# Kernel tuning notes

Measured on AMD Instinct MI355X. Metric: run time of the kernel, lower is better.

Reference implementation:

```python
import jax, jax.numpy as jnp
import numpy as np

B, S, IN = 1024, 256, 8
H = 512
F = 96  # forecast_len
OUT = 1


def _lstm_step(h, c, x, Wih, Whh, bih, bhh):
    # PyTorch gate order: i, f, g, o
    gates = x @ Wih.T + h @ Whh.T + (bih + bhh)  # [B, 4H]
    i, f, g, o = jnp.split(gates, 4, axis=-1)
    i = jax.nn.sigmoid(i)
    f = jax.nn.sigmoid(f)
    g = jnp.tanh(g)
    o = jax.nn.sigmoid(o)
    c_new = f * c + i * g
    h_new = o * jnp.tanh(c_new)
    return h_new, c_new


def setup_inputs() -> dict:
    key = jax.random.key(0)
    ks = jax.random.split(key, 12)
    s_in = 1.0 / np.sqrt(H)
    def u(k, shape):
        return jax.random.uniform(k, shape, jnp.float32, -s_in, s_in)
    return {
        "x": jax.random.normal(ks[0], (B, S, IN), jnp.float32),
        "enc_Wih": u(ks[1], (4 * H, IN)),
        "enc_Whh": u(ks[2], (4 * H, H)),
        "enc_bih": u(ks[3], (4 * H,)),
        "enc_bhh": u(ks[4], (4 * H,)),
        "dec_Wih": u(ks[5], (4 * H, OUT)),
        "dec_Whh": u(ks[6], (4 * H, H)),
        "dec_bih": u(ks[7], (4 * H,)),
        "dec_bhh": u(ks[8], (4 * H,)),
        "out_W": u(ks[9], (OUT, H)),
        "out_b": u(ks[10], (OUT,)),
    }


def reference(x, enc_Wih, enc_Whh, enc_bih, enc_bhh,
              dec_Wih, dec_Whh, dec_bih, dec_bhh, out_W, out_b):
    batch = x.shape[0]
    h0 = jnp.zeros((batch, H), x.dtype)
    c0 = jnp.zeros((batch, H), x.dtype)

    # ---- Encoder: scan over time ----
    def enc_step(carry, xt):
        h, c = carry
        h, c = _lstm_step(h, c, xt, enc_Wih, enc_Whh, enc_bih, enc_bhh)
        return (h, c), None

    xs = jnp.swapaxes(x, 0, 1)  # [S, B, IN]
    (h, c), _ = jax.lax.scan(enc_step, (h0, c0), xs)

    y0 = jnp.zeros((batch, OUT), x.dtype)

    def dec_step(carry, _):
        h, c, y = carry
        h, c = _lstm_step(h, c, y, dec_Wih, dec_Whh, dec_bih, dec_bhh)
        pred = h @ out_W.T + out_b  # [B, 1]
        return (h, c, pred), pred

    _, preds = jax.lax.scan(dec_step, (h, c, y0), None, length=F)  # [F, B, 1]
    return jnp.swapaxes(preds[..., 0], 0, 1)  # [B, F]
```

## Files before the change

kernel.cpp:

```cpp
#include <hip/hip_runtime.h>


#define Hh 512
#define K2 544
#define BATCH 1024
#define SEQ 256
#define FCAST 96
#define Mrows 64
#define SAS 552
#define SHS 40

typedef _Float16 f16;
typedef _Float16 f16x8 __attribute__((ext_vector_type(8)));
typedef float f32x4 __attribute__((ext_vector_type(4)));

__device__ __forceinline__ float sigf(float v) { return 1.0f / (1.0f + __expf(-v)); }
__device__ __forceinline__ float tanhf_(float v) { return 1.0f - 2.0f / (__expf(2.0f * v) + 1.0f); }

__device__ __forceinline__ f16x8 ld16(const f16* p, bool byp) {
  f16x8 d;
  if (byp) asm volatile("global_load_dwordx4 %0, %1, off sc0 sc1" : "=v"(d) : "v"(p) : "memory");
  else     asm volatile("global_load_dwordx4 %0, %1, off sc0"     : "=v"(d) : "v"(p) : "memory");
  return d;
}
__device__ __forceinline__ void st16(f16* p, f16x8 v, bool byp) {
  if (byp) asm volatile("global_store_dwordx4 %0, %1, off sc0 sc1" :: "v"(p), "v"(v) : "memory");
  else     asm volatile("global_store_dwordx4 %0, %1, off"         :: "v"(p), "v"(v) : "memory");
}
__device__ __forceinline__ int atomic_add_l2(int* p, int v) {
  int old;
  asm volatile("global_atomic_add %0, %1, %2, off sc0\n\ts_waitcnt vmcnt(0)"
               : "=v"(old) : "v"(p), "v"(v) : "memory");
  return old;
}

__global__ void prep_weights(const float* __restrict__ encWih, const float* __restrict__ encWhh,
                             const float* __restrict__ decWih, const float* __restrict__ decWhh,
                             const float* __restrict__ encBih, const float* __restrict__ encBhh,
                             const float* __restrict__ decBih, const float* __restrict__ decBhh,
                             const float* __restrict__ outW, const float* __restrict__ outB,
                             f16* __restrict__ encT, f16* __restrict__ decPW, f16* __restrict__ decFW,
                             float* __restrict__ bE, float* __restrict__ bP, float* __restrict__ bF) {
  int id = blockIdx.x * 256 + threadIdx.x;
  if (id >= 2048 * 68) return;
  int n = id / 68, c8 = id % 68;
  int nslot = n >> 7, c = n & 127, w = c >> 5, cc = c & 31, ct = cc >> 4, l4v = cc & 15;
  int g = ct * 2 + (l4v >> 3), j = l4v & 7;
  int unit = nslot * 32 + w * 8 + j, r = g * Hh + unit;
  size_t o = (size_t)n * K2 + c8 * 8;
  if (c8 < 64) {
    float dwih = decWih[r];
#pragma unroll
    for (int e = 0; e < 8; ++e) {
      int k = c8 * 8 + e;
      encT[o + e] = (f16)encWhh[(size_t)r * Hh + k];
      float dw = decWhh[(size_t)r * Hh + k];
      decPW[o + e] = (f16)dw;
      decFW[o + e] = (f16)(dw + outW[k] * dwih);
    }
  } else if (c8 == 64) {
#pragma unroll
    for (int e = 0; e < 8; ++e) {
      encT[o + e] = (f16)encWih[r * 8 + e];
      decPW[o + e] = (f16)0.f;
      decFW[o + e] = (f16)0.f;
    }
  } else {
#pragma unroll
    for (int e = 0; e < 8; ++e) {
      encT[o + e] = (f16)0.f;
      decPW[o + e] = (f16)0.f;
      decFW[o + e] = (f16)0.f;
    }
  }
  if (c8 == 0) {
    bE[n] = encBih[r] + encBhh[r];
    float bd = decBih[r] + decBhh[r];
    bP[n] = bd;
    bF[n] = bd + outB[0] * decWih[r];
  }
}

__global__ void init_state(f16* __restrict__ h0, float* __restrict__ out,
                           const float* __restrict__ outB, int* __restrict__ sync) {
  int i = blockIdx.x * 256 + threadIdx.x;
  if (i < BATCH * Hh) h0[i] = (f16)0.f;
  if (i < BATCH * FCAST) out[i] = outB[0];
  if (i < 2048) sync[i] = 0;
}

__global__ __launch_bounds__(256, 1) void lstm_persist(
    const f16* __restrict__ encT, const f16* __restrict__ decPW, const f16* __restrict__ decFW,
    const float* __restrict__ bE, const float* __restrict__ bP, const float* __restrict__ bF,
    const float* __restrict__ x, f16* __restrict__ h0, f16* __restrict__ h1,
    float* __restrict__ out, const float* __restrict__ outW, int* __restrict__ sync) {
  __shared__ __align__(16) f16 sA[Mrows * SAS];
  __shared__ __align__(16) f16 sH[Mrows * SHS];
  __shared__ int sInfo[2];

  int* cnt = sync;
  int* slots = sync + 1024;
  int* arrive = sync + 1032;

  const int T = threadIdx.x;
  const int w = T >> 6, lane = T & 63, l4 = lane & 15, q = lane >> 4;
  const int j = l4 & 7;
  const bool lo = (l4 < 8);

  int xcd;
  asm("s_getreg_b32 %0, hwreg(HW_REG_XCC_ID)" : "=s"(xcd));
  xcd &= 7;

  if (T == 0) {
    int r = __hip_atomic_fetch_add(&slots[xcd], 1, __ATOMIC_RELAXED, __HIP_MEMORY_SCOPE_AGENT);
    sInfo[0] = r;
    __hip_atomic_fetch_add(arrive, 1, __ATOMIC_RELAXED, __HIP_MEMORY_SCOPE_AGENT);
    while (__hip_atomic_load(arrive, __ATOMIC_RELAXED, __HIP_MEMORY_SCOPE_AGENT) < 256)
      __builtin_amdgcn_s_sleep(2);
    int ok = 1;
    for (int xx = 0; xx < 8; ++xx)
      ok &= (__hip_atomic_load(&slots[xx], __ATOMIC_RELAXED, __HIP_MEMORY_SCOPE_AGENT) == 32);
    sInfo[1] = ok;
  }
  __syncthreads();
  const int rank = sInfo[0];
  const bool uni = (sInfo[1] != 0);
  int group, nslot;
  if (uni) { group = xcd * 2 + (rank >> 4); nslot = rank & 15; }
  else     { group = (int)blockIdx.x >> 4;  nslot = (int)blockIdx.x & 15; }
  const int m0 = group * Mrows, n0 = nslot * 128, u0 = nslot * 32;
  int* myCnt = cnt + group * 32;

  f16x8 bw[2][17];
  float bias_r[4];
  float cst[2][4];
#pragma unroll
  for (int a = 0; a < 2; ++a)
#pragma unroll
    for (int r = 0; r < 4; ++r) cst[a][r] = 0.f;

  const int myUnit = u0 + w * 8 + j;

  auto loadB = [&](const f16* WT, const float* bias) {
#pragma unroll
    for (int ct = 0; ct < 2; ++ct) {
      const f16* base = &WT[(size_t)(n0 + w * 32 + ct * 16 + l4) * K2 + q * 8];
#pragma unroll
      for (int ks = 0; ks < 17; ++ks) bw[ct][ks] = *(const f16x8*)(base + ks * 32);
    }
#pragma unroll
    for (int g = 0; g < 4; ++g)
      bias_r[g] = bias[n0 + w * 32 + (g >> 1) * 16 + (g & 1) * 8 + j];
  };

  loadB(encT, bE);
  float ow_r = 0.f;

  for (int s = 0; s < SEQ + FCAST; ++s) {
    const bool enc = s < SEQ;
    if (s == SEQ) {
      loadB(decPW, bP);
      ow_r = outW[myUnit];
    } else if (s == SEQ + 1) {
      loadB(decFW, bF);
    }

    if (s > 0) {
      asm volatile("s_waitcnt vmcnt(0)" ::: "memory");
      __syncthreads();
      if (T == 0) {
        if (uni) {
          atomic_add_l2(myCnt, 1);
          while (atomic_add_l2(myCnt, 0) < 16 * s) __builtin_amdgcn_s_sleep(1);
        } else {
          __hip_atomic_fetch_add(myCnt, 1, __ATOMIC_RELAXED, __HIP_MEMORY_SCOPE_AGENT);
          while (__hip_atomic_load(myCnt, __ATOMIC_RELAXED, __HIP_MEMORY_SCOPE_AGENT) < 16 * s)
            __builtin_amdgcn_s_sleep(2);
        }
      }
      __syncthreads();
    }

    const f16* hin = (s & 1) ? h1 : h0;
    f16* hout = (s & 1) ? h0 : h1;

    f16x8 d[16];
#pragma unroll
    for (int jj = 0; jj < 16; ++jj) {
      int id = T + 256 * jj;
      int row = id >> 6, c8 = (id & 63) * 8;
      d[jj] = ld16(&hin[(size_t)(m0 + row) * Hh + c8], !uni);
    }
    const bool hasx = enc && (T < Mrows);
    float4 xa, xb;
    if (hasx) {
      const float* xp = &x[((size_t)(m0 + T) * SEQ + s) * 8];
      xa = *(const float4*)xp;
      xb = *(const float4*)(xp + 4);
    }
    asm volatile("s_waitcnt vmcnt(8)" ::: "memory");
#pragma unroll
    for (int jj = 0; jj < 8; ++jj) {
      int id = T + 256 * jj;
      int row = id >> 6, c8 = (id & 63) * 8;
      *(f16x8*)&sA[row * SAS + c8] = d[jj];
    }
    __syncthreads();

    f32x4 acc[4][2];
#pragma unroll
    for (int a = 0; a < 4; ++a)
#pragma unroll
      for (int c = 0; c < 2; ++c) acc[a][c] = (f32x4){0.f, 0.f, 0.f, 0.f};

    auto mac = [&](int at, int ks) {
      int ko = ks * 32 + q * 8;
      f16x8 af = *(const f16x8*)&sA[(at * 16 + l4) * SAS + ko];
      acc[at][0] = __builtin_amdgcn_mfma_f32_16x16x32_f16(af, bw[0][ks], acc[at][0], 0, 0, 0);
      acc[at][1] = __builtin_amdgcn_mfma_f32_16x16x32_f16(af, bw[1][ks], acc[at][1], 0, 0, 0);
    };
#pragma unroll
    for (int ks = 0; ks < 16; ++ks) {
      mac(0, ks);
      mac(1, ks);
    }

    asm volatile("s_waitcnt vmcnt(0)" ::: "memory");
#pragma unroll
    for (int jj = 8; jj < 16; ++jj) {
      int id = T + 256 * jj;
      int row = id >> 6, c8 = (id & 63) * 8;
      *(f16x8*)&sA[row * SAS + c8] = d[jj];
    }
    if (hasx) {
      f16x8 xv = {(f16)xa.x, (f16)xa.y, (f16)xa.z, (f16)xa.w,
                  (f16)xb.x, (f16)xb.y, (f16)xb.z, (f16)xb.w};
      f16x8 z = {(f16)0.f, (f16)0.f, (f16)0.f, (f16)0.f, (f16)0.f, (f16)0.f, (f16)0.f, (f16)0.f};
      *(f16x8*)&sA[T * SAS + 512] = xv;
      *(f16x8*)&sA[T * SAS + 520] = z;
      *(f16x8*)&sA[T * SAS + 528] = z;
      *(f16x8*)&sA[T * SAS + 536] = z;
    }
    __syncthreads();

    if (enc) {
      mac(0, 16);
      mac(1, 16);
    }
#pragma unroll
    for (int ks = 0; ks < 16; ++ks) {
      mac(2, ks);
      mac(3, ks);
    }
    if (enc) {
      mac(2, 16);
      mac(3, 16);
    }

#pragma unroll
    for (int ah = 0; ah < 2; ++ah) {
#pragma unroll
      for (int r = 0; r < 4; ++r) {
        int atL = ah;
        int atH = ah + 2;
        float xiL = acc[atL][0][r], xgL = acc[atL][1][r];
        float xiH = acc[atH][0][r], xgH = acc[atH][1][r];
        float payload0 = lo ? xiH : xiL;
        float payload1 = lo ? xgH : xgL;
        float pf_recv = __shfl_xor(payload0, 8, 16);
        float po_recv = __shfl_xor(payload1, 8, 16);
        float gi = lo ? xiL : pf_recv;
        float gf = lo ? pf_recv : xiH;
        float gg_ = lo ? xgL : po_recv;
        float go = lo ? po_recv : xgH;
        float pi = gi + bias_r[0];
        float pf = gf + bias_r[1];
        float pg = gg_ + bias_r[2];
        float po = go + bias_r[3];
        float ig = sigf(pi), fg = sigf(pf), gg = tanhf_(pg), og = sigf(po);
        float cn = fg * cst[ah][r] + ig * gg;
        cst[ah][r] = cn;
        float hn = og * tanhf_(cn);
        int at = lo ? atL : atH;
        int row = at * 16 + q * 4 + r;
        sH[row * SHS + w * 8 + j] = (f16)hn;
        if (!enc) {
          float pp = hn * ow_r;
          pp += __shfl_xor(pp, 1, 16);
          pp += __shfl_xor(pp, 2, 16);
          pp += __shfl_xor(pp, 4, 16);
          if (j == 0) atomicAdd(&out[(m0 + row) * FCAST + (s - SEQ)], pp);
        }
      }
    }
    __syncthreads();

    {
      int row = T >> 2, seg = T & 3;
      f16x8 hv = *(const f16x8*)&sH[row * SHS + seg * 8];
      st16(&hout[(size_t)(m0 + row) * Hh + u0 + seg * 8], hv, !uni);
    }
  }
}

extern "C" void kernel_launch(void* const* d_in, const int* in_sizes, int n_in, void* d_out,
                              int out_size, void* d_ws, size_t ws_size, hipStream_t stream) {
  const float* x = (const float*)d_in[0];
  const float* encWih = (const float*)d_in[1];
  const float* encWhh = (const float*)d_in[2];
  const float* encBih = (const float*)d_in[3];
  const float* encBhh = (const float*)d_in[4];
  const float* decWih = (const float*)d_in[5];
  const float* decWhh = (const float*)d_in[6];
  const float* decBih = (const float*)d_in[7];
  const float* decBhh = (const float*)d_in[8];
  const float* outW = (const float*)d_in[9];
  const float* outB = (const float*)d_in[10];
  float* out = (float*)d_out;

  char* ws = (char*)d_ws;
  f16* encT = (f16*)ws;
  f16* decPW = encT + 2048 * K2;
  f16* decFW = decPW + 2048 * K2;
  f16* h0 = decFW + 2048 * K2;
  f16* h1 = h0 + BATCH * Hh;
  float* bE = (float*)(h1 + BATCH * Hh);
  float* bP = bE + 2048;
  float* bF = bP + 2048;
  int* sync = (int*)(bF + 2048);

  prep_weights<<<544, 256, 0, stream>>>(encWih, encWhh, decWih, decWhh, encBih, encBhh, decBih,
                                        decBhh, outW, outB, encT, decPW, decFW, bE, bP, bF);
  init_state<<<2048, 256, 0, stream>>>(h0, out, outB, sync);
  lstm_persist<<<256, 256, 0, stream>>>(encT, decPW, decFW, bE, bP, bF, x, h0, h1, out, outW, sync);
}
```

Measured before the change: 2.451 ms.

## Prefetch next-step x across barrier and swizzle LDS A-tile columns

The load of the next timestep's x input is moved to the end of the current step, so it overlaps the inter-block barrier. Wave 0 now waits with vmcnt(2) so these two loads can stay outstanding. The h tile stored into LDS gets an XOR-like rotation of its 8-element column groups, with matching reads, to cut bank conflicts on the MFMA A-operand loads. It also adds release/acquire ordering on the startup barrier and zeroes h1 at init, which adds a little init work.

```diff
diff --git a/kernel.cpp b/kernel.cpp
--- a/kernel.cpp
+++ b/kernel.cpp
@@ -81,10 +81,10 @@
   }
 }
 
-__global__ void init_state(f16* __restrict__ h0, float* __restrict__ out,
+__global__ void init_state(f16* __restrict__ h0, f16* __restrict__ h1, float* __restrict__ out,
                            const float* __restrict__ outB, int* __restrict__ sync) {
   int i = blockIdx.x * 256 + threadIdx.x;
-  if (i < BATCH * Hh) h0[i] = (f16)0.f;
+  if (i < BATCH * Hh) { h0[i] = (f16)0.f; h1[i] = (f16)0.f; }
   if (i < BATCH * FCAST) out[i] = outB[0];
   if (i < 2048) sync[i] = 0;
 }
@@ -106,6 +106,7 @@
   const int w = T >> 6, lane = T & 63, l4 = lane & 15, q = lane >> 4;
   const int j = l4 & 7;
   const bool lo = (l4 < 8);
+  const int qr8 = ((q + l4) & 3) << 3;
 
   int xcd;
   asm("s_getreg_b32 %0, hwreg(HW_REG_XCC_ID)" : "=s"(xcd));
@@ -114,9 +115,10 @@
   if (T == 0) {
     int r = __hip_atomic_fetch_add(&slots[xcd], 1, __ATOMIC_RELAXED, __HIP_MEMORY_SCOPE_AGENT);
     sInfo[0] = r;
-    __hip_atomic_fetch_add(arrive, 1, __ATOMIC_RELAXED, __HIP_MEMORY_SCOPE_AGENT);
-    while (__hip_atomic_load(arrive, __ATOMIC_RELAXED, __HIP_MEMORY_SCOPE_AGENT) < 256)
+    __hip_atomic_fetch_add(arrive, 1, __ATOMIC_RELEASE, __HIP_MEMORY_SCOPE_AGENT);
+    while (__hip_atomic_load(arrive, __ATOMIC_ACQUIRE, __HIP_MEMORY_SCOPE_AGENT) < 256)
       __builtin_amdgcn_s_sleep(2);
+    __threadfence();
     int ok = 1;
     for (int xx = 0; xx < 8; ++xx)
       ok &= (__hip_atomic_load(&slots[xx], __ATOMIC_RELAXED, __HIP_MEMORY_SCOPE_AGENT) == 32);
@@ -156,6 +158,13 @@
   loadB(encT, bE);
   float ow_r = 0.f;
 
+  float4 xa, xb;
+  if (T < Mrows) {
+    const float* xp = &x[((size_t)(m0 + T) * SEQ + 0) * 8];
+    xa = *(const float4*)xp;
+    xb = *(const float4*)(xp + 4);
+  }
+
   for (int s = 0; s < SEQ + FCAST; ++s) {
     const bool enc = s < SEQ;
     if (s == SEQ) {
@@ -166,7 +175,8 @@
     }
 
     if (s > 0) {
-      asm volatile("s_waitcnt vmcnt(0)" ::: "memory");
+      if (s < SEQ && w == 0) asm volatile("s_waitcnt vmcnt(2)" ::: "memory");
+      else                   asm volatile("s_waitcnt vmcnt(0)" ::: "memory");
       __syncthreads();
       if (T == 0) {
         if (uni) {
@@ -191,19 +201,13 @@
       int row = id >> 6, c8 = (id & 63) * 8;
       d[jj] = ld16(&hin[(size_t)(m0 + row) * Hh + c8], !uni);
     }
-    const bool hasx = enc && (T < Mrows);
-    float4 xa, xb;
-    if (hasx) {
-      const float* xp = &x[((size_t)(m0 + T) * SEQ + s) * 8];
-      xa = *(const float4*)xp;
-      xb = *(const float4*)(xp + 4);
-    }
     asm volatile("s_waitcnt vmcnt(8)" ::: "memory");
 #pragma unroll
     for (int jj = 0; jj < 8; ++jj) {
       int id = T + 256 * jj;
       int row = id >> 6, c8 = (id & 63) * 8;
-      *(f16x8*)&sA[row * SAS + c8] = d[jj];
+      int csw = (c8 & ~31) | ((((c8 >> 3) + row) & 3) << 3);
+      *(f16x8*)&sA[row * SAS + csw] = d[jj];
     }
     __syncthreads();
 
@@ -214,7 +218,7 @@
       for (int c = 0; c < 2; ++c) acc[a][c] = (f32x4){0.f, 0.f, 0.f, 0.f};
 
     auto mac = [&](int at, int ks) {
-      int ko = ks * 32 + q * 8;
+      int ko = (ks < 16) ? (ks * 32 + qr8) : (512 + q * 8);
       f16x8 af = *(const f16x8*)&sA[(at * 16 + l4) * SAS + ko];
       acc[at][0] = __builtin_amdgcn_mfma_f32_16x16x32_f16(af, bw[0][ks], acc[at][0], 0, 0, 0);
       acc[at][1] = __builtin_amdgcn_mfma_f32_16x16x32_f16(af, bw[1][ks], acc[at][1], 0, 0, 0);
@@ -230,9 +234,10 @@
     for (int jj = 8; jj < 16; ++jj) {
       int id = T + 256 * jj;
       int row = id >> 6, c8 = (id & 63) * 8;
-      *(f16x8*)&sA[row * SAS + c8] = d[jj];
-    }
-    if (hasx) {
+      int csw = (c8 & ~31) | ((((c8 >> 3) + row) & 3) << 3);
+      *(f16x8*)&sA[row * SAS + csw] = d[jj];
+    }
+    if (enc && T < Mrows) {
       f16x8 xv = {(f16)xa.x, (f16)xa.y, (f16)xa.z, (f16)xa.w,
                   (f16)xb.x, (f16)xb.y, (f16)xb.z, (f16)xb.w};
       f16x8 z = {(f16)0.f, (f16)0.f, (f16)0.f, (f16)0.f, (f16)0.f, (f16)0.f, (f16)0.f, (f16)0.f};
@@ -300,6 +305,12 @@
       f16x8 hv = *(const f16x8*)&sH[row * SHS + seg * 8];
       st16(&hout[(size_t)(m0 + row) * Hh + u0 + seg * 8], hv, !uni);
     }
+
+    if (s + 1 < SEQ && T < Mrows) {
+      const float* xp = &x[((size_t)(m0 + T) * SEQ + (s + 1)) * 8];
+      xa = *(const float4*)xp;
+      xb = *(const float4*)(xp + 4);
+    }
   }
 }
 
@@ -331,6 +342,6 @@
 
   prep_weights<<<544, 256, 0, stream>>>(encWih, encWhh, decWih, decWhh, encBih, encBhh, decBih,
                                         decBhh, outW, outB, encT, decPW, decFW, bE, bP, bF);
-  init_state<<<2048, 256, 0, stream>>>(h0, out, outB, sync);
+  init_state<<<2048, 256, 0, stream>>>(h0, h1, out, outB, sync);
   lstm_persist<<<256, 256, 0, stream>>>(encT, decPW, decFW, bE, bP, bF, x, h0, h1, out, outW, sync);
 }
```

Measured after the change: 2.377 ms. 1.03x faster.
